# Performance work log

Measured on AMD Instinct MI355X. Metric: run time of the kernel, lower is better.

## Reference

```python
import jax, jax.numpy as jnp
import numpy as np

H_HEADS = 16
STATE_N = 64

def setup_inputs() -> dict:
    key = jax.random.key(0)
    ks = jax.random.split(key, 9)
    B, T, D = 2, 1024, 1024
    H, ch, N = H_HEADS, D // H_HEADS, STATE_N
    inp = jax.random.normal(ks[0], (B, T, D), dtype=jnp.float32)
    # lin_logA params scaled so exp(cumsum(logA)) stays bounded (decaying state)
    W_logA = jax.random.normal(ks[1], (H, 1, ch), dtype=jnp.float32) * 0.01
    b_logA = jnp.full((H, 1), -0.05, dtype=jnp.float32)
    W_XBC = jax.random.normal(ks[3], (H, ch + 2 * N, ch), dtype=jnp.float32) * (1.0 / np.sqrt(ch))
    b_XBC = jax.random.normal(ks[4], (H, ch + 2 * N), dtype=jnp.float32) * 0.02
    W_gate = jax.random.normal(ks[5], (H, ch, ch), dtype=jnp.float32) * (1.0 / np.sqrt(ch))
    b_gate = jax.random.normal(ks[6], (H, ch), dtype=jnp.float32) * 0.02
    W_out = jax.random.normal(ks[7], (D, D), dtype=jnp.float32) * (1.0 / np.sqrt(D))
    b_out = jax.random.normal(ks[8], (D,), dtype=jnp.float32) * 0.02
    return {"inp": inp, "W_logA": W_logA, "b_logA": b_logA, "W_XBC": W_XBC,
            "b_XBC": b_XBC, "W_gate": W_gate, "b_gate": b_gate,
            "W_out": W_out, "b_out": b_out}

def _mamba2_forward(inp, W_logA, b_logA, W_XBC, b_XBC, W_gate, b_gate, W_out, b_out):
    B, T, D = inp.shape
    H, N = H_HEADS, STATE_N
    ch = D // H
    x = inp.reshape(B, T, H, ch)  # B,T,H,ch
    # MultiheadLinear: matmul((H,out,in), x[...,None]) + bias
    logA = jnp.einsum('hoc,bthc->btho', W_logA, x)[..., 0] + b_logA[:, 0]  # B,T,H
    XBC = jax.nn.silu(jnp.einsum('hoc,bthc->btho', W_XBC, x) + b_XBC)     # B,T,H,ch+2N
    X = XBC[..., :ch]                 # B,T,H,ch
    Bm = XBC[..., ch:ch + N]          # B,T,H,N
    Cm = XBC[..., ch + N:]            # B,T,H,N
    # quadratic SSM: A_ss[b,h,i,j] = exp(cum[i]-cum[j]) for j<=i else 0
    cum = jnp.cumsum(jnp.swapaxes(logA, 1, 2), axis=-1)  # B,H,T
    diff = cum[..., :, None] - cum[..., None, :]          # B,H,T,T
    causal = jnp.tril(jnp.ones((T, T), dtype=bool))
    A_ss = jnp.where(causal, jnp.exp(jnp.where(causal, diff, 0.0)), 0.0)  # B,H,T,T
    G = jnp.einsum('bihn,bjhn->bhij', Cm, Bm)             # B,H,T,T (C_i . B_j)
    Y = jnp.einsum('bhij,bjhc->bihc', A_ss * G, X)        # B,T,H,ch
    gate = jnp.einsum('hoc,bthc->btho', W_gate, x) + b_gate
    Yg = (gate * Y).reshape(B, T, D)
    return Yg @ W_out.T + b_out

def reference(inp, W_logA, b_logA, W_XBC, b_XBC, W_gate, b_gate, W_out, b_out):
    return _mamba2_forward(inp, W_logA, b_logA, W_XBC, b_XBC, W_gate, b_gate, W_out, b_out)
```

## Files before the change

### kernel.cpp

```cpp
#include <hip/hip_runtime.h>

typedef unsigned int   u32;
typedef unsigned short u16;
typedef __attribute__((ext_vector_type(8))) short bf16x8;
typedef __attribute__((ext_vector_type(4))) float f32x4;

__device__ __forceinline__ float bfs(u16 u) {
  union { u32 i; float f; } v; v.i = ((u32)u) << 16; return v.f;
}
__device__ __forceinline__ u16 f2bf(float f) {
  union { float f; u32 i; } v; v.f = f;
  u32 r = v.i + 0x7fffu + ((v.i >> 16) & 1u);
  return (u16)(r >> 16);
}
__device__ __forceinline__ ushort4 f2bf4(float4 v) {
  ushort4 p; p.x = f2bf(v.x); p.y = f2bf(v.y); p.z = f2bf(v.z); p.w = f2bf(v.w);
  return p;
}

__global__ __launch_bounds__(256) void k_proj(
    const float* __restrict__ inp,
    const float* __restrict__ W_XBC,  const float* __restrict__ b_XBC,
    const float* __restrict__ W_gate, const float* __restrict__ b_gate,
    const float* __restrict__ W_logA, const float* __restrict__ b_logA,
    const float* __restrict__ Wout, u16* __restrict__ WoutB,
    u16* __restrict__ XsT, u16* __restrict__ Bms, u16* __restrict__ Cms,
    u16* __restrict__ gatesP, float* __restrict__ lexp, float* __restrict__ linv,
    float* __restrict__ decArr, float* __restrict__ G)
{
  int tt = blockIdx.x, h = blockIdx.y;
  int tid = threadIdx.x;
  int w = tid >> 6, l = tid & 63, q = l >> 4, lr = l & 15;
  int m0 = tt * 64;
  int b = m0 >> 10, tl0 = m0 & 1023;
  int bh = b * 16 + h;
  int jt = tt & 15;

  __shared__ u16 Xt[64][72];
  __shared__ u16 Wt[256][72];
  __shared__ float wl[64];
  __shared__ float sg[64];

  {
    int fid = h * 32 + tt;
    const float4* src = (const float4*)Wout + (size_t)fid * 512;
    ushort4* dst = (ushort4*)WoutB + (size_t)fid * 512;
    for (int i = tid; i < 512; i += 256) dst[i] = f2bf4(src[i]);
  }

  if (tid < 64) wl[tid] = W_logA[h * 64 + tid];
#pragma unroll
  for (int i = 0; i < 4; ++i) {
    int f = tid + 256 * i; int r = f >> 4, cq = f & 15;
    float4 xv = *(const float4*)(inp + (size_t)(m0 + r) * 1024 + h * 64 + 4 * cq);
    *(ushort4*)&Xt[r][4 * cq] = f2bf4(xv);
  }
#pragma unroll
  for (int i = 0; i < 16; ++i) {
    int f = tid + 256 * i; int r = f >> 4, cq = f & 15;
    const float* ws = (r < 192) ? (W_XBC + ((size_t)h * 192 + r) * 64)
                                : (W_gate + ((size_t)h * 64 + (r - 192)) * 64);
    *(ushort4*)&Wt[r][4 * cq] = f2bf4(*(const float4*)(ws + 4 * cq));
  }
  __syncthreads();

  bf16x8 af[4][2];
#pragma unroll
  for (int rt = 0; rt < 4; ++rt) {
    af[rt][0] = *(const bf16x8*)&Xt[16 * rt + lr][q * 8];
    af[rt][1] = *(const bf16x8*)&Xt[16 * rt + lr][32 + q * 8];
  }

  f32x4 acc[4][4];
#pragma unroll
  for (int rt = 0; rt < 4; ++rt)
#pragma unroll
    for (int ct = 0; ct < 4; ++ct) acc[rt][ct] = (f32x4){0.f, 0.f, 0.f, 0.f};

#pragma unroll
  for (int ct = 0; ct < 4; ++ct) {
    bf16x8 b0 = *(const bf16x8*)&Wt[64 * w + 16 * ct + lr][q * 8];
    bf16x8 b1 = *(const bf16x8*)&Wt[64 * w + 16 * ct + lr][32 + q * 8];
#pragma unroll
    for (int rt = 0; rt < 4; ++rt) {
      acc[rt][ct] = __builtin_amdgcn_mfma_f32_16x16x32_bf16(af[rt][0], b0, acc[rt][ct], 0, 0, 0);
      acc[rt][ct] = __builtin_amdgcn_mfma_f32_16x16x32_bf16(af[rt][1], b1, acc[rt][ct], 0, 0, 0);
    }
  }

  if (tid < 64) {
    float a = b_logA[h];
#pragma unroll 16
    for (int k = 0; k < 64; ++k) a += bfs(Xt[tid][k]) * wl[k];
    float lv = a;
#pragma unroll
    for (int off = 1; off < 64; off <<= 1) {
      float n = __shfl_up(lv, off, 64);
      if (tid >= off) lv += n;
    }
    float L = __shfl(lv, 63, 64);
    sg[tid] = __expf(L - lv);
    lexp[(size_t)bh * 1024 + tl0 + tid] = __expf(lv);
    linv[(size_t)bh * 1024 + tl0 + tid] = __expf(-lv);
    if (tid == 63) decArr[bh * 16 + jt] = __expf(L);
  }

  if (w < 3) {
#pragma unroll
    for (int ct = 0; ct < 4; ++ct) {
      float bias = b_XBC[h * 192 + 64 * w + 16 * ct + lr];
#pragma unroll
      for (int rt = 0; rt < 4; ++rt)
#pragma unroll
        for (int r = 0; r < 4; ++r) {
          float s = acc[rt][ct][r] + bias;
          acc[rt][ct][r] = s / (1.f + __expf(-s));
        }
    }
  } else {
#pragma unroll
    for (int ct = 0; ct < 4; ++ct) {
      float bias = b_gate[h * 64 + 16 * ct + lr];
#pragma unroll
      for (int rt = 0; rt < 4; ++rt)
#pragma unroll
        for (int r = 0; r < 4; ++r) acc[rt][ct][r] += bias;
    }
  }
  __syncthreads();

  {
#pragma unroll
    for (int ct = 0; ct < 4; ++ct)
#pragma unroll
      for (int rt = 0; rt < 4; ++rt)
#pragma unroll
        for (int r = 0; r < 4; ++r) {
          int t = 16 * rt + 4 * q + r, n = 16 * ct + lr;
          u16 v = f2bf(acc[rt][ct][r]);
          if (w == 0) {
            Wt[n][t] = v;
          } else if (w == 1) {
            Wt[64 + n][t] = v;
            Xt[t][n] = v;
          } else if (w == 2) {
            Wt[128 + t][n] = v;
          } else {
            Wt[192 + t][n] = v;
          }
        }
  }
  __syncthreads();

  {
#pragma unroll
    for (int i = 0; i < 16; ++i) {
      int s = l + 64 * i; int row = s >> 4, cq = s & 15;
      if (w == 0) {
        ushort4 v = *(ushort4*)&Wt[row][4 * cq];
        *(ushort4*)(XsT + ((size_t)bh * 64 + row) * 1024 + tl0 + 4 * cq) = v;
      } else if (w == 1) {
        ushort4 v = *(ushort4*)&Xt[row][4 * cq];
        *(ushort4*)(Bms + ((size_t)bh * 1024 + tl0 + row) * 64 + 4 * cq) = v;
      } else if (w == 2) {
        ushort4 v = *(ushort4*)&Wt[128 + row][4 * cq];
        *(ushort4*)(Cms + ((size_t)bh * 1024 + tl0 + row) * 64 + 4 * cq) = v;
      } else {
        ushort4 v = *(ushort4*)&Wt[192 + row][4 * cq];
        *(ushort4*)(gatesP + ((size_t)bh * 1024 + tl0 + row) * 64 + 4 * cq) = v;
      }
    }
  }

  {
    bf16x8 a0r = *(const bf16x8*)&Wt[16 * w + lr][q * 8];
    bf16x8 a1r = *(const bf16x8*)&Wt[16 * w + lr][32 + q * 8];
    bf16x8 a0, a1;
#pragma unroll
    for (int jj = 0; jj < 8; ++jj) {
      a0[jj] = (short)f2bf(bfs((u16)a0r[jj]) * sg[q * 8 + jj]);
      a1[jj] = (short)f2bf(bfs((u16)a1r[jj]) * sg[32 + q * 8 + jj]);
    }
    f32x4 gacc[4];
#pragma unroll
    for (int nt = 0; nt < 4; ++nt) {
      gacc[nt] = (f32x4){0.f, 0.f, 0.f, 0.f};
      bf16x8 bb0 = *(const bf16x8*)&Wt[64 + 16 * nt + lr][q * 8];
      bf16x8 bb1 = *(const bf16x8*)&Wt[64 + 16 * nt + lr][32 + q * 8];
      gacc[nt] = __builtin_amdgcn_mfma_f32_16x16x32_bf16(a0, bb0, gacc[nt], 0, 0, 0);
      gacc[nt] = __builtin_amdgcn_mfma_f32_16x16x32_bf16(a1, bb1, gacc[nt], 0, 0, 0);
    }
    float* Gt = G + ((size_t)bh * 16 + jt) * 4096;
#pragma unroll
    for (int nt = 0; nt < 4; ++nt)
#pragma unroll
      for (int r = 0; r < 4; ++r)
        Gt[(16 * w + 4 * q + r) * 64 + 16 * nt + lr] = gacc[nt][r];
  }
}

__global__ __launch_bounds__(256) void k_mid(
    const float* __restrict__ G, const float* __restrict__ decArr,
    u16* __restrict__ HpreT)
{
  int cc = blockIdx.x, bh = blockIdx.y;
  int tid = threadIdx.x;
  int e = cc * 256 + tid;
  __shared__ float dsm[16];
  if (tid < 16) dsm[tid] = decArr[bh * 16 + tid];
  __syncthreads();
  const float* Gb = G + (size_t)bh * 16 * 4096 + e;
  float g[16];
#pragma unroll
  for (int jtl = 0; jtl < 16; ++jtl) g[jtl] = Gb[(size_t)jtl * 4096];
  u16* Hb = HpreT + (size_t)bh * 16 * 4096 + e;
  float hst = 0.f;
#pragma unroll
  for (int jtl = 0; jtl < 16; ++jtl) {
    Hb[(size_t)jtl * 4096] = f2bf(hst);
    hst = dsm[jtl] * hst + g[jtl];
  }
}

__global__ __launch_bounds__(256) void k_ssm2(
    const u16* __restrict__ XsT, const u16* __restrict__ Bms,
    const u16* __restrict__ Cms,
    const float* __restrict__ lexp, const float* __restrict__ linv,
    const u16* __restrict__ HpreT, const u16* __restrict__ gatesP,
    u16* __restrict__ Yg)
{
  int it = blockIdx.x, bh = blockIdx.y;
  int b = bh >> 4, h = bh & 15;
  int tid = threadIdx.x;
  int w = tid >> 6, l = tid & 63, q = l >> 4, lr = l & 15;
  int i0 = it * 64;

  __shared__ u16 Cts[64][72];
  __shared__ u16 Bts[64][72];
  __shared__ u16 Xts[64][72];
  __shared__ u16 HTt[64][72];
  __shared__ u16 Sts[64][72];
  __shared__ float ref_[64], cef[64];

  const u16* Xb = XsT + (size_t)bh * 64 * 1024;
  const u16* Bb = Bms + (size_t)bh * 64 * 1024;
  const u16* Cb = Cms + (size_t)bh * 64 * 1024;
  const u16* Hb = HpreT + ((size_t)bh * 16 + it) * 4096;
  const u16* Gb = gatesP + ((size_t)bh * 1024 + i0) * 64;

#pragma unroll
  for (int i = 0; i < 4; ++i) {
    int f = tid + 256 * i; int r = f >> 4, cq = f & 15;
    *(ushort4*)&Xts[r][4 * cq] = *(const ushort4*)(Xb + (size_t)r * 1024 + i0 + 4 * cq);
    *(ushort4*)&HTt[r][4 * cq] = *(const ushort4*)(Hb + r * 64 + 4 * cq);
    *(ushort4*)&Bts[r][4 * cq] = *(const ushort4*)(Bb + (size_t)(i0 + r) * 64 + 4 * cq);
    *(ushort4*)&Cts[r][4 * cq] = *(const ushort4*)(Cb + (size_t)(i0 + r) * 64 + 4 * cq);
  }
  if (tid < 64) {
    ref_[tid] = lexp[(size_t)bh * 1024 + i0 + tid];
    cef[tid]  = linv[(size_t)bh * 1024 + i0 + tid];
  }
  __syncthreads();

  bf16x8 ca0 = *(const bf16x8*)&Cts[16 * w + lr][q * 8];
  bf16x8 ca1 = *(const bf16x8*)&Cts[16 * w + lr][32 + q * 8];

#pragma unroll
  for (int ct = 0; ct < 4; ++ct) {
    f32x4 s = (f32x4){0.f, 0.f, 0.f, 0.f};
    bf16x8 b0 = *(const bf16x8*)&Bts[16 * ct + lr][q * 8];
    bf16x8 b1 = *(const bf16x8*)&Bts[16 * ct + lr][32 + q * 8];
    s = __builtin_amdgcn_mfma_f32_16x16x32_bf16(ca0, b0, s, 0, 0, 0);
    s = __builtin_amdgcn_mfma_f32_16x16x32_bf16(ca1, b1, s, 0, 0, 0);
    int jl = 16 * ct + lr;
    float cj = cef[jl];
#pragma unroll
    for (int r = 0; r < 4; ++r) {
      int il = 16 * w + q * 4 + r;
      float v = (jl > il) ? 0.f : s[r] * ref_[il] * cj;
      Sts[il][jl] = f2bf(v);
    }
  }

  bf16x8 sa0 = *(const bf16x8*)&Sts[16 * w + lr][q * 8];
  bf16x8 sa1 = *(const bf16x8*)&Sts[16 * w + lr][32 + q * 8];
  f32x4 accd[4], acco[4];
#pragma unroll
  for (int ct = 0; ct < 4; ++ct) {
    accd[ct] = (f32x4){0.f, 0.f, 0.f, 0.f};
    acco[ct] = (f32x4){0.f, 0.f, 0.f, 0.f};
    bf16x8 x0 = *(const bf16x8*)&Xts[16 * ct + lr][q * 8];
    bf16x8 x1 = *(const bf16x8*)&Xts[16 * ct + lr][32 + q * 8];
    accd[ct] = __builtin_amdgcn_mfma_f32_16x16x32_bf16(sa0, x0, accd[ct], 0, 0, 0);
    accd[ct] = __builtin_amdgcn_mfma_f32_16x16x32_bf16(sa1, x1, accd[ct], 0, 0, 0);
    bf16x8 h0 = *(const bf16x8*)&HTt[16 * ct + lr][q * 8];
    bf16x8 h1 = *(const bf16x8*)&HTt[16 * ct + lr][32 + q * 8];
    acco[ct] = __builtin_amdgcn_mfma_f32_16x16x32_bf16(ca0, h0, acco[ct], 0, 0, 0);
    acco[ct] = __builtin_amdgcn_mfma_f32_16x16x32_bf16(ca1, h1, acco[ct], 0, 0, 0);
  }

  __syncthreads();

#pragma unroll
  for (int ct = 0; ct < 4; ++ct) {
    int c = 16 * ct + lr;
#pragma unroll
    for (int r = 0; r < 4; ++r) {
      int il = 16 * w + q * 4 + r;
      float y = accd[ct][r] + ref_[il] * acco[ct][r];
      Xts[il][c] = f2bf(y);
    }
  }
  __syncthreads();

#pragma unroll
  for (int i = 0; i < 4; ++i) {
    int f = tid + 256 * i; int r = f >> 4, cq = f & 15;
    ushort4 yv = *(ushort4*)&Xts[r][4 * cq];
    ushort4 gv = *(const ushort4*)(Gb + (size_t)r * 64 + 4 * cq);
    ushort4 o;
    o.x = f2bf(bfs(yv.x) * bfs(gv.x));
    o.y = f2bf(bfs(yv.y) * bfs(gv.y));
    o.z = f2bf(bfs(yv.z) * bfs(gv.z));
    o.w = f2bf(bfs(yv.w) * bfs(gv.w));
    *(ushort4*)(Yg + ((size_t)(b * 1024 + i0 + r)) * 1024 + h * 64 + 4 * cq) = o;
  }
}

__global__ __launch_bounds__(512) void k_out(
    const u16* __restrict__ Yg, const u16* __restrict__ WoutB,
    const float* __restrict__ bout, float* __restrict__ out)
{
  int bm = blockIdx.x, bn = blockIdx.y;
  int tid = threadIdx.x;
  int w = tid >> 6, l = tid & 63, q = l >> 4, lr = l & 15;
  int m0 = bm * 128, d0 = bn * 64;

  __shared__ u16 Yt[128][72];
  __shared__ u16 Wt[64][72];

  f32x4 acc[4];
#pragma unroll
  for (int ct = 0; ct < 4; ++ct) acc[ct] = (f32x4){0.f, 0.f, 0.f, 0.f};

  ushort4 py[4], pw[2];
#pragma unroll
  for (int i = 0; i < 4; ++i) {
    int f = tid + 512 * i; int r = f >> 4, cq = f & 15;
    py[i] = *(const ushort4*)(Yg + (size_t)(m0 + r) * 1024 + 4 * cq);
  }
#pragma unroll
  for (int i = 0; i < 2; ++i) {
    int f = tid + 512 * i; int r = f >> 4, cq = f & 15;
    pw[i] = *(const ushort4*)(WoutB + (size_t)(d0 + r) * 1024 + 4 * cq);
  }

  for (int kt = 0; kt < 16; ++kt) {
    __syncthreads();
#pragma unroll
    for (int i = 0; i < 4; ++i) {
      int f = tid + 512 * i; int r = f >> 4, cq = f & 15;
      *(ushort4*)&Yt[r][4 * cq] = py[i];
    }
#pragma unroll
    for (int i = 0; i < 2; ++i) {
      int f = tid + 512 * i; int r = f >> 4, cq = f & 15;
      *(ushort4*)&Wt[r][4 * cq] = pw[i];
    }
    __syncthreads();

    if (kt < 15) {
      int k1 = (kt + 1) * 64;
#pragma unroll
      for (int i = 0; i < 4; ++i) {
        int f = tid + 512 * i; int r = f >> 4, cq = f & 15;
        py[i] = *(const ushort4*)(Yg + (size_t)(m0 + r) * 1024 + k1 + 4 * cq);
      }
#pragma unroll
      for (int i = 0; i < 2; ++i) {
        int f = tid + 512 * i; int r = f >> 4, cq = f & 15;
        pw[i] = *(const ushort4*)(WoutB + (size_t)(d0 + r) * 1024 + k1 + 4 * cq);
      }
    }

    bf16x8 a0 = *(const bf16x8*)&Yt[16 * w + lr][q * 8];
    bf16x8 a1 = *(const bf16x8*)&Yt[16 * w + lr][32 + q * 8];
#pragma unroll
    for (int ct = 0; ct < 4; ++ct) {
      bf16x8 b0 = *(const bf16x8*)&Wt[16 * ct + lr][q * 8];
      bf16x8 b1 = *(const bf16x8*)&Wt[16 * ct + lr][32 + q * 8];
      acc[ct] = __builtin_amdgcn_mfma_f32_16x16x32_bf16(a0, b0, acc[ct], 0, 0, 0);
      acc[ct] = __builtin_amdgcn_mfma_f32_16x16x32_bf16(a1, b1, acc[ct], 0, 0, 0);
    }
  }

#pragma unroll
  for (int ct = 0; ct < 4; ++ct) {
    int d = d0 + 16 * ct + lr;
    float bo = bout[d];
#pragma unroll
    for (int r = 0; r < 4; ++r) {
      int m = m0 + 16 * w + q * 4 + r;
      out[(size_t)m * 1024 + d] = acc[ct][r] + bo;
    }
  }
}

extern "C" void kernel_launch(void* const* d_in, const int* in_sizes, int n_in,
                              void* d_out, int out_size, void* d_ws, size_t ws_size,
                              hipStream_t stream)
{
  const float* inp   = (const float*)d_in[0];
  const float* WlogA = (const float*)d_in[1];
  const float* blogA = (const float*)d_in[2];
  const float* WXBC  = (const float*)d_in[3];
  const float* bXBC  = (const float*)d_in[4];
  const float* Wgate = (const float*)d_in[5];
  const float* bgate = (const float*)d_in[6];
  const float* Wout  = (const float*)d_in[7];
  const float* bout  = (const float*)d_in[8];
  float* out = (float*)d_out;

  const size_t SZ = (size_t)2 * 16 * 1024 * 64;
  float* lexp   = (float*)d_ws;
  float* linv   = lexp + 32768;
  float* decA   = linv + 32768;
  float* G      = decA + 512;
  u16* base16 = (u16*)(G + (size_t)32 * 16 * 4096);
  u16* XsT    = base16;
  u16* Bms    = XsT + SZ;
  u16* Cms    = Bms + SZ;
  u16* gatesP = Cms + SZ;
  u16* Yg     = gatesP + SZ;
  u16* WoutB  = Yg + SZ;
  u16* HpreT  = WoutB + 1024 * 1024;

  k_proj<<<dim3(32, 16), 256, 0, stream>>>(inp, WXBC, bXBC, Wgate, bgate,
                                           WlogA, blogA, Wout, WoutB,
                                           XsT, Bms, Cms, gatesP,
                                           lexp, linv, decA, G);
  k_mid<<<dim3(16, 32), 256, 0, stream>>>(G, decA, HpreT);
  k_ssm2<<<dim3(16, 32), 256, 0, stream>>>(XsT, Bms, Cms, lexp, linv,
                                           HpreT, gatesP, Yg);
  k_out<<<dim3(16, 16), 512, 0, stream>>>(Yg, WoutB, bout, out);
}
```

Before: 125.4 us.

## Fuse all four kernels into one persistent kernel with grid barriers

Merges projection, chunk-state scan, SSM and output GEMM into a single 512-block kernel separated by atomic grid-wide barriers. XBC, B, C and gate tiles stay in shared memory between phases instead of round-tripping through global buffers, and three extra launches are removed. The output GEMM is retiled to 64x64 per 256-thread block to match the fused grid. This relies on all 512 blocks being co-resident (launch_bounds 256,2) and adds spin-wait barrier overhead plus a memset launch.

```diff
diff --git a/kernel.cpp b/kernel.cpp
--- a/kernel.cpp
+++ b/kernel.cpp
@@ -18,28 +18,43 @@
   return p;
 }
 
-__global__ __launch_bounds__(256) void k_proj(
+#define NBLK 512u
+
+__device__ __forceinline__ void gridbar(u32* cnt, int idx) {
+  __threadfence();
+  __syncthreads();
+  if (threadIdx.x == 0) {
+    __hip_atomic_fetch_add(&cnt[idx], 1u, __ATOMIC_ACQ_REL, __HIP_MEMORY_SCOPE_AGENT);
+    while (__hip_atomic_load(&cnt[idx], __ATOMIC_ACQUIRE, __HIP_MEMORY_SCOPE_AGENT) < NBLK) {}
+  }
+  __syncthreads();
+  __threadfence();
+}
+
+__global__ __launch_bounds__(256, 2) void k_fused(
     const float* __restrict__ inp,
     const float* __restrict__ W_XBC,  const float* __restrict__ b_XBC,
     const float* __restrict__ W_gate, const float* __restrict__ b_gate,
     const float* __restrict__ W_logA, const float* __restrict__ b_logA,
-    const float* __restrict__ Wout, u16* __restrict__ WoutB,
-    u16* __restrict__ XsT, u16* __restrict__ Bms, u16* __restrict__ Cms,
-    u16* __restrict__ gatesP, float* __restrict__ lexp, float* __restrict__ linv,
-    float* __restrict__ decArr, float* __restrict__ G)
+    const float* __restrict__ Wout,   const float* __restrict__ bout,
+    u32* __restrict__ bar,
+    u16* __restrict__ WoutB, float* __restrict__ decArr,
+    float* __restrict__ G, u16* __restrict__ HpreT,
+    u16* __restrict__ Yg, float* __restrict__ out)
 {
-  int tt = blockIdx.x, h = blockIdx.y;
-  int tid = threadIdx.x;
-  int w = tid >> 6, l = tid & 63, q = l >> 4, lr = l & 15;
-  int m0 = tt * 64;
-  int b = m0 >> 10, tl0 = m0 & 1023;
-  int bh = b * 16 + h;
-  int jt = tt & 15;
+  const int tt = blockIdx.x, h = blockIdx.y;
+  const int tid = threadIdx.x;
+  const int w = tid >> 6, l = tid & 63, q = l >> 4, lr = l & 15;
+  const int m0 = tt * 64;
+  const int b = tt >> 4;
+  const int bh = b * 16 + h;
+  const int it = tt & 15;
 
   __shared__ u16 Xt[64][72];
   __shared__ u16 Wt[256][72];
   __shared__ float wl[64];
   __shared__ float sg[64];
+  __shared__ float ref_[64], cef[64];
 
   {
     int fid = h * 32 + tt;
@@ -64,72 +79,72 @@
   }
   __syncthreads();
 
-  bf16x8 af[4][2];
-#pragma unroll
-  for (int rt = 0; rt < 4; ++rt) {
-    af[rt][0] = *(const bf16x8*)&Xt[16 * rt + lr][q * 8];
-    af[rt][1] = *(const bf16x8*)&Xt[16 * rt + lr][32 + q * 8];
-  }
-
-  f32x4 acc[4][4];
-#pragma unroll
-  for (int rt = 0; rt < 4; ++rt)
-#pragma unroll
-    for (int ct = 0; ct < 4; ++ct) acc[rt][ct] = (f32x4){0.f, 0.f, 0.f, 0.f};
-
-#pragma unroll
-  for (int ct = 0; ct < 4; ++ct) {
-    bf16x8 b0 = *(const bf16x8*)&Wt[64 * w + 16 * ct + lr][q * 8];
-    bf16x8 b1 = *(const bf16x8*)&Wt[64 * w + 16 * ct + lr][32 + q * 8];
+  {
+    bf16x8 af[4][2];
 #pragma unroll
     for (int rt = 0; rt < 4; ++rt) {
-      acc[rt][ct] = __builtin_amdgcn_mfma_f32_16x16x32_bf16(af[rt][0], b0, acc[rt][ct], 0, 0, 0);
-      acc[rt][ct] = __builtin_amdgcn_mfma_f32_16x16x32_bf16(af[rt][1], b1, acc[rt][ct], 0, 0, 0);
-    }
-  }
-
-  if (tid < 64) {
-    float a = b_logA[h];
+      af[rt][0] = *(const bf16x8*)&Xt[16 * rt + lr][q * 8];
+      af[rt][1] = *(const bf16x8*)&Xt[16 * rt + lr][32 + q * 8];
+    }
+
+    f32x4 acc[4][4];
+#pragma unroll
+    for (int rt = 0; rt < 4; ++rt)
+#pragma unroll
+      for (int ct = 0; ct < 4; ++ct) acc[rt][ct] = (f32x4){0.f, 0.f, 0.f, 0.f};
+
+#pragma unroll
+    for (int ct = 0; ct < 4; ++ct) {
+      bf16x8 b0 = *(const bf16x8*)&Wt[64 * w + 16 * ct + lr][q * 8];
+      bf16x8 b1 = *(const bf16x8*)&Wt[64 * w + 16 * ct + lr][32 + q * 8];
+#pragma unroll
+      for (int rt = 0; rt < 4; ++rt) {
+        acc[rt][ct] = __builtin_amdgcn_mfma_f32_16x16x32_bf16(af[rt][0], b0, acc[rt][ct], 0, 0, 0);
+        acc[rt][ct] = __builtin_amdgcn_mfma_f32_16x16x32_bf16(af[rt][1], b1, acc[rt][ct], 0, 0, 0);
+      }
+    }
+
+    if (tid < 64) {
+      float a = b_logA[h];
 #pragma unroll 16
-    for (int k = 0; k < 64; ++k) a += bfs(Xt[tid][k]) * wl[k];
-    float lv = a;
-#pragma unroll
-    for (int off = 1; off < 64; off <<= 1) {
-      float n = __shfl_up(lv, off, 64);
-      if (tid >= off) lv += n;
-    }
-    float L = __shfl(lv, 63, 64);
-    sg[tid] = __expf(L - lv);
-    lexp[(size_t)bh * 1024 + tl0 + tid] = __expf(lv);
-    linv[(size_t)bh * 1024 + tl0 + tid] = __expf(-lv);
-    if (tid == 63) decArr[bh * 16 + jt] = __expf(L);
-  }
-
-  if (w < 3) {
-#pragma unroll
-    for (int ct = 0; ct < 4; ++ct) {
-      float bias = b_XBC[h * 192 + 64 * w + 16 * ct + lr];
-#pragma unroll
-      for (int rt = 0; rt < 4; ++rt)
-#pragma unroll
-        for (int r = 0; r < 4; ++r) {
-          float s = acc[rt][ct][r] + bias;
-          acc[rt][ct][r] = s / (1.f + __expf(-s));
-        }
-    }
-  } else {
-#pragma unroll
-    for (int ct = 0; ct < 4; ++ct) {
-      float bias = b_gate[h * 64 + 16 * ct + lr];
-#pragma unroll
-      for (int rt = 0; rt < 4; ++rt)
-#pragma unroll
-        for (int r = 0; r < 4; ++r) acc[rt][ct][r] += bias;
-    }
-  }
-  __syncthreads();
-
-  {
+      for (int k = 0; k < 64; ++k) a += bfs(Xt[tid][k]) * wl[k];
+      float lv = a;
+#pragma unroll
+      for (int off = 1; off < 64; off <<= 1) {
+        float n = __shfl_up(lv, off, 64);
+        if (tid >= off) lv += n;
+      }
+      float L = __shfl(lv, 63, 64);
+      sg[tid]   = __expf(L - lv);
+      ref_[tid] = __expf(lv);
+      cef[tid]  = __expf(-lv);
+      if (tid == 63) decArr[bh * 16 + it] = __expf(L);
+    }
+
+    if (w < 3) {
+#pragma unroll
+      for (int ct = 0; ct < 4; ++ct) {
+        float bias = b_XBC[h * 192 + 64 * w + 16 * ct + lr];
+#pragma unroll
+        for (int rt = 0; rt < 4; ++rt)
+#pragma unroll
+          for (int r = 0; r < 4; ++r) {
+            float s = acc[rt][ct][r] + bias;
+            acc[rt][ct][r] = s / (1.f + __expf(-s));
+          }
+      }
+    } else {
+#pragma unroll
+      for (int ct = 0; ct < 4; ++ct) {
+        float bias = b_gate[h * 64 + 16 * ct + lr];
+#pragma unroll
+        for (int rt = 0; rt < 4; ++rt)
+#pragma unroll
+          for (int r = 0; r < 4; ++r) acc[rt][ct][r] += bias;
+      }
+    }
+    __syncthreads();
+
 #pragma unroll
     for (int ct = 0; ct < 4; ++ct)
 #pragma unroll
@@ -149,259 +164,190 @@
             Wt[192 + t][n] = v;
           }
         }
-  }
-  __syncthreads();
-
-  {
-#pragma unroll
-    for (int i = 0; i < 16; ++i) {
-      int s = l + 64 * i; int row = s >> 4, cq = s & 15;
-      if (w == 0) {
-        ushort4 v = *(ushort4*)&Wt[row][4 * cq];
-        *(ushort4*)(XsT + ((size_t)bh * 64 + row) * 1024 + tl0 + 4 * cq) = v;
-      } else if (w == 1) {
-        ushort4 v = *(ushort4*)&Xt[row][4 * cq];
-        *(ushort4*)(Bms + ((size_t)bh * 1024 + tl0 + row) * 64 + 4 * cq) = v;
-      } else if (w == 2) {
-        ushort4 v = *(ushort4*)&Wt[128 + row][4 * cq];
-        *(ushort4*)(Cms + ((size_t)bh * 1024 + tl0 + row) * 64 + 4 * cq) = v;
-      } else {
-        ushort4 v = *(ushort4*)&Wt[192 + row][4 * cq];
-        *(ushort4*)(gatesP + ((size_t)bh * 1024 + tl0 + row) * 64 + 4 * cq) = v;
-      }
-    }
-  }
-
-  {
-    bf16x8 a0r = *(const bf16x8*)&Wt[16 * w + lr][q * 8];
-    bf16x8 a1r = *(const bf16x8*)&Wt[16 * w + lr][32 + q * 8];
-    bf16x8 a0, a1;
-#pragma unroll
-    for (int jj = 0; jj < 8; ++jj) {
-      a0[jj] = (short)f2bf(bfs((u16)a0r[jj]) * sg[q * 8 + jj]);
-      a1[jj] = (short)f2bf(bfs((u16)a1r[jj]) * sg[32 + q * 8 + jj]);
-    }
-    f32x4 gacc[4];
-#pragma unroll
-    for (int nt = 0; nt < 4; ++nt) {
-      gacc[nt] = (f32x4){0.f, 0.f, 0.f, 0.f};
-      bf16x8 bb0 = *(const bf16x8*)&Wt[64 + 16 * nt + lr][q * 8];
-      bf16x8 bb1 = *(const bf16x8*)&Wt[64 + 16 * nt + lr][32 + q * 8];
-      gacc[nt] = __builtin_amdgcn_mfma_f32_16x16x32_bf16(a0, bb0, gacc[nt], 0, 0, 0);
-      gacc[nt] = __builtin_amdgcn_mfma_f32_16x16x32_bf16(a1, bb1, gacc[nt], 0, 0, 0);
-    }
-    float* Gt = G + ((size_t)bh * 16 + jt) * 4096;
-#pragma unroll
-    for (int nt = 0; nt < 4; ++nt)
-#pragma unroll
-      for (int r = 0; r < 4; ++r)
-        Gt[(16 * w + 4 * q + r) * 64 + 16 * nt + lr] = gacc[nt][r];
-  }
-}
-
-__global__ __launch_bounds__(256) void k_mid(
-    const float* __restrict__ G, const float* __restrict__ decArr,
-    u16* __restrict__ HpreT)
-{
-  int cc = blockIdx.x, bh = blockIdx.y;
-  int tid = threadIdx.x;
-  int e = cc * 256 + tid;
-  __shared__ float dsm[16];
-  if (tid < 16) dsm[tid] = decArr[bh * 16 + tid];
-  __syncthreads();
-  const float* Gb = G + (size_t)bh * 16 * 4096 + e;
-  float g[16];
-#pragma unroll
-  for (int jtl = 0; jtl < 16; ++jtl) g[jtl] = Gb[(size_t)jtl * 4096];
-  u16* Hb = HpreT + (size_t)bh * 16 * 4096 + e;
-  float hst = 0.f;
-#pragma unroll
-  for (int jtl = 0; jtl < 16; ++jtl) {
-    Hb[(size_t)jtl * 4096] = f2bf(hst);
-    hst = dsm[jtl] * hst + g[jtl];
-  }
-}
-
-__global__ __launch_bounds__(256) void k_ssm2(
-    const u16* __restrict__ XsT, const u16* __restrict__ Bms,
-    const u16* __restrict__ Cms,
-    const float* __restrict__ lexp, const float* __restrict__ linv,
-    const u16* __restrict__ HpreT, const u16* __restrict__ gatesP,
-    u16* __restrict__ Yg)
-{
-  int it = blockIdx.x, bh = blockIdx.y;
-  int b = bh >> 4, h = bh & 15;
-  int tid = threadIdx.x;
-  int w = tid >> 6, l = tid & 63, q = l >> 4, lr = l & 15;
-  int i0 = it * 64;
-
-  __shared__ u16 Cts[64][72];
-  __shared__ u16 Bts[64][72];
-  __shared__ u16 Xts[64][72];
-  __shared__ u16 HTt[64][72];
-  __shared__ u16 Sts[64][72];
-  __shared__ float ref_[64], cef[64];
-
-  const u16* Xb = XsT + (size_t)bh * 64 * 1024;
-  const u16* Bb = Bms + (size_t)bh * 64 * 1024;
-  const u16* Cb = Cms + (size_t)bh * 64 * 1024;
-  const u16* Hb = HpreT + ((size_t)bh * 16 + it) * 4096;
-  const u16* Gb = gatesP + ((size_t)bh * 1024 + i0) * 64;
-
-#pragma unroll
-  for (int i = 0; i < 4; ++i) {
-    int f = tid + 256 * i; int r = f >> 4, cq = f & 15;
-    *(ushort4*)&Xts[r][4 * cq] = *(const ushort4*)(Xb + (size_t)r * 1024 + i0 + 4 * cq);
-    *(ushort4*)&HTt[r][4 * cq] = *(const ushort4*)(Hb + r * 64 + 4 * cq);
-    *(ushort4*)&Bts[r][4 * cq] = *(const ushort4*)(Bb + (size_t)(i0 + r) * 64 + 4 * cq);
-    *(ushort4*)&Cts[r][4 * cq] = *(const ushort4*)(Cb + (size_t)(i0 + r) * 64 + 4 * cq);
-  }
-  if (tid < 64) {
-    ref_[tid] = lexp[(size_t)bh * 1024 + i0 + tid];
-    cef[tid]  = linv[(size_t)bh * 1024 + i0 + tid];
-  }
-  __syncthreads();
-
-  bf16x8 ca0 = *(const bf16x8*)&Cts[16 * w + lr][q * 8];
-  bf16x8 ca1 = *(const bf16x8*)&Cts[16 * w + lr][32 + q * 8];
-
-#pragma unroll
-  for (int ct = 0; ct < 4; ++ct) {
-    f32x4 s = (f32x4){0.f, 0.f, 0.f, 0.f};
-    bf16x8 b0 = *(const bf16x8*)&Bts[16 * ct + lr][q * 8];
-    bf16x8 b1 = *(const bf16x8*)&Bts[16 * ct + lr][32 + q * 8];
-    s = __builtin_amdgcn_mfma_f32_16x16x32_bf16(ca0, b0, s, 0, 0, 0);
-    s = __builtin_amdgcn_mfma_f32_16x16x32_bf16(ca1, b1, s, 0, 0, 0);
-    int jl = 16 * ct + lr;
-    float cj = cef[jl];
-#pragma unroll
-    for (int r = 0; r < 4; ++r) {
-      int il = 16 * w + q * 4 + r;
-      float v = (jl > il) ? 0.f : s[r] * ref_[il] * cj;
-      Sts[il][jl] = f2bf(v);
-    }
-  }
-
-  bf16x8 sa0 = *(const bf16x8*)&Sts[16 * w + lr][q * 8];
-  bf16x8 sa1 = *(const bf16x8*)&Sts[16 * w + lr][32 + q * 8];
-  f32x4 accd[4], acco[4];
-#pragma unroll
-  for (int ct = 0; ct < 4; ++ct) {
-    accd[ct] = (f32x4){0.f, 0.f, 0.f, 0.f};
-    acco[ct] = (f32x4){0.f, 0.f, 0.f, 0.f};
-    bf16x8 x0 = *(const bf16x8*)&Xts[16 * ct + lr][q * 8];
-    bf16x8 x1 = *(const bf16x8*)&Xts[16 * ct + lr][32 + q * 8];
-    accd[ct] = __builtin_amdgcn_mfma_f32_16x16x32_bf16(sa0, x0, accd[ct], 0, 0, 0);
-    accd[ct] = __builtin_amdgcn_mfma_f32_16x16x32_bf16(sa1, x1, accd[ct], 0, 0, 0);
-    bf16x8 h0 = *(const bf16x8*)&HTt[16 * ct + lr][q * 8];
-    bf16x8 h1 = *(const bf16x8*)&HTt[16 * ct + lr][32 + q * 8];
-    acco[ct] = __builtin_amdgcn_mfma_f32_16x16x32_bf16(ca0, h0, acco[ct], 0, 0, 0);
-    acco[ct] = __builtin_amdgcn_mfma_f32_16x16x32_bf16(ca1, h1, acco[ct], 0, 0, 0);
-  }
-
-  __syncthreads();
-
-#pragma unroll
-  for (int ct = 0; ct < 4; ++ct) {
-    int c = 16 * ct + lr;
-#pragma unroll
-    for (int r = 0; r < 4; ++r) {
-      int il = 16 * w + q * 4 + r;
-      float y = accd[ct][r] + ref_[il] * acco[ct][r];
-      Xts[il][c] = f2bf(y);
-    }
-  }
-  __syncthreads();
-
-#pragma unroll
-  for (int i = 0; i < 4; ++i) {
-    int f = tid + 256 * i; int r = f >> 4, cq = f & 15;
-    ushort4 yv = *(ushort4*)&Xts[r][4 * cq];
-    ushort4 gv = *(const ushort4*)(Gb + (size_t)r * 64 + 4 * cq);
-    ushort4 o;
-    o.x = f2bf(bfs(yv.x) * bfs(gv.x));
-    o.y = f2bf(bfs(yv.y) * bfs(gv.y));
-    o.z = f2bf(bfs(yv.z) * bfs(gv.z));
-    o.w = f2bf(bfs(yv.w) * bfs(gv.w));
-    *(ushort4*)(Yg + ((size_t)(b * 1024 + i0 + r)) * 1024 + h * 64 + 4 * cq) = o;
-  }
-}
-
-__global__ __launch_bounds__(512) void k_out(
-    const u16* __restrict__ Yg, const u16* __restrict__ WoutB,
-    const float* __restrict__ bout, float* __restrict__ out)
-{
-  int bm = blockIdx.x, bn = blockIdx.y;
-  int tid = threadIdx.x;
-  int w = tid >> 6, l = tid & 63, q = l >> 4, lr = l & 15;
-  int m0 = bm * 128, d0 = bn * 64;
-
-  __shared__ u16 Yt[128][72];
-  __shared__ u16 Wt[64][72];
-
-  f32x4 acc[4];
-#pragma unroll
-  for (int ct = 0; ct < 4; ++ct) acc[ct] = (f32x4){0.f, 0.f, 0.f, 0.f};
-
-  ushort4 py[4], pw[2];
-#pragma unroll
-  for (int i = 0; i < 4; ++i) {
-    int f = tid + 512 * i; int r = f >> 4, cq = f & 15;
-    py[i] = *(const ushort4*)(Yg + (size_t)(m0 + r) * 1024 + 4 * cq);
-  }
-#pragma unroll
-  for (int i = 0; i < 2; ++i) {
-    int f = tid + 512 * i; int r = f >> 4, cq = f & 15;
-    pw[i] = *(const ushort4*)(WoutB + (size_t)(d0 + r) * 1024 + 4 * cq);
-  }
-
-  for (int kt = 0; kt < 16; ++kt) {
-    __syncthreads();
+    __syncthreads();
+
+    {
+      bf16x8 a0r = *(const bf16x8*)&Wt[16 * w + lr][q * 8];
+      bf16x8 a1r = *(const bf16x8*)&Wt[16 * w + lr][32 + q * 8];
+      bf16x8 a0, a1;
+#pragma unroll
+      for (int jj = 0; jj < 8; ++jj) {
+        a0[jj] = (short)f2bf(bfs((u16)a0r[jj]) * sg[q * 8 + jj]);
+        a1[jj] = (short)f2bf(bfs((u16)a1r[jj]) * sg[32 + q * 8 + jj]);
+      }
+      f32x4 gacc[4];
+#pragma unroll
+      for (int nt = 0; nt < 4; ++nt) {
+        gacc[nt] = (f32x4){0.f, 0.f, 0.f, 0.f};
+        bf16x8 bb0 = *(const bf16x8*)&Wt[64 + 16 * nt + lr][q * 8];
+        bf16x8 bb1 = *(const bf16x8*)&Wt[64 + 16 * nt + lr][32 + q * 8];
+        gacc[nt] = __builtin_amdgcn_mfma_f32_16x16x32_bf16(a0, bb0, gacc[nt], 0, 0, 0);
+        gacc[nt] = __builtin_amdgcn_mfma_f32_16x16x32_bf16(a1, bb1, gacc[nt], 0, 0, 0);
+      }
+      float* Gt = G + ((size_t)bh * 16 + it) * 4096;
+#pragma unroll
+      for (int nt = 0; nt < 4; ++nt)
+#pragma unroll
+        for (int r = 0; r < 4; ++r)
+          Gt[(16 * w + 4 * q + r) * 64 + 16 * nt + lr] = gacc[nt][r];
+    }
+  }
+
+  gridbar(bar, 0);
+
+  {
+    int fb = (h << 5) | tt;
+    int bh2 = fb >> 4;
+    int e = ((fb & 15) << 8) + tid;
+    if (tid < 16) wl[tid] = decArr[bh2 * 16 + tid];
+    __syncthreads();
+    const float* Gb = G + (size_t)bh2 * 16 * 4096 + e;
+    u16* Hb = HpreT + (size_t)bh2 * 16 * 4096 + e;
+    float gv[16];
+#pragma unroll
+    for (int j = 0; j < 16; ++j) gv[j] = Gb[(size_t)j * 4096];
+    float hst = 0.f;
+#pragma unroll
+    for (int j = 0; j < 16; ++j) {
+      Hb[(size_t)j * 4096] = f2bf(hst);
+      hst = wl[j] * hst + gv[j];
+    }
+  }
+
+  gridbar(bar, 1);
+
+  {
+    const u16* Hb = HpreT + ((size_t)bh * 16 + it) * 4096;
+
+    u16 (*Xts)[72] = (u16 (*)[72])&Wt[0];
+    u16 (*Sts)[72] = (u16 (*)[72])&Wt[64];
+    u16 (*Cts)[72] = (u16 (*)[72])&Wt[128];
+    u16 (*Gts)[72] = (u16 (*)[72])&Wt[192];
+
+    bf16x8 ca0 = *(const bf16x8*)&Cts[16 * w + lr][q * 8];
+    bf16x8 ca1 = *(const bf16x8*)&Cts[16 * w + lr][32 + q * 8];
+
+#pragma unroll
+    for (int ct = 0; ct < 4; ++ct) {
+      f32x4 s = (f32x4){0.f, 0.f, 0.f, 0.f};
+      bf16x8 b0 = *(const bf16x8*)&Xt[16 * ct + lr][q * 8];
+      bf16x8 b1 = *(const bf16x8*)&Xt[16 * ct + lr][32 + q * 8];
+      s = __builtin_amdgcn_mfma_f32_16x16x32_bf16(ca0, b0, s, 0, 0, 0);
+      s = __builtin_amdgcn_mfma_f32_16x16x32_bf16(ca1, b1, s, 0, 0, 0);
+      int jl = 16 * ct + lr;
+      float cj = cef[jl];
+#pragma unroll
+      for (int r = 0; r < 4; ++r) {
+        int il = 16 * w + q * 4 + r;
+        float v = (jl > il) ? 0.f : s[r] * ref_[il] * cj;
+        Sts[il][jl] = f2bf(v);
+      }
+    }
+
+    bf16x8 sa0 = *(const bf16x8*)&Sts[16 * w + lr][q * 8];
+    bf16x8 sa1 = *(const bf16x8*)&Sts[16 * w + lr][32 + q * 8];
+    f32x4 accd[4], acco[4];
+#pragma unroll
+    for (int ct = 0; ct < 4; ++ct) {
+      accd[ct] = (f32x4){0.f, 0.f, 0.f, 0.f};
+      acco[ct] = (f32x4){0.f, 0.f, 0.f, 0.f};
+      bf16x8 x0 = *(const bf16x8*)&Xts[16 * ct + lr][q * 8];
+      bf16x8 x1 = *(const bf16x8*)&Xts[16 * ct + lr][32 + q * 8];
+      accd[ct] = __builtin_amdgcn_mfma_f32_16x16x32_bf16(sa0, x0, accd[ct], 0, 0, 0);
+      accd[ct] = __builtin_amdgcn_mfma_f32_16x16x32_bf16(sa1, x1, accd[ct], 0, 0, 0);
+      bf16x8 h0 = *(const bf16x8*)(Hb + (size_t)(16 * ct + lr) * 64 + q * 8);
+      bf16x8 h1 = *(const bf16x8*)(Hb + (size_t)(16 * ct + lr) * 64 + 32 + q * 8);
+      acco[ct] = __builtin_amdgcn_mfma_f32_16x16x32_bf16(ca0, h0, acco[ct], 0, 0, 0);
+      acco[ct] = __builtin_amdgcn_mfma_f32_16x16x32_bf16(ca1, h1, acco[ct], 0, 0, 0);
+    }
+
+    __syncthreads();
+
+#pragma unroll
+    for (int ct = 0; ct < 4; ++ct) {
+      int c = 16 * ct + lr;
+#pragma unroll
+      for (int r = 0; r < 4; ++r) {
+        int il = 16 * w + q * 4 + r;
+        float y = accd[ct][r] + ref_[il] * acco[ct][r];
+        Xts[il][c] = f2bf(y);
+      }
+    }
+    __syncthreads();
+
 #pragma unroll
     for (int i = 0; i < 4; ++i) {
-      int f = tid + 512 * i; int r = f >> 4, cq = f & 15;
-      *(ushort4*)&Yt[r][4 * cq] = py[i];
-    }
-#pragma unroll
-    for (int i = 0; i < 2; ++i) {
-      int f = tid + 512 * i; int r = f >> 4, cq = f & 15;
-      *(ushort4*)&Wt[r][4 * cq] = pw[i];
-    }
-    __syncthreads();
-
-    if (kt < 15) {
-      int k1 = (kt + 1) * 64;
+      int f = tid + 256 * i; int r = f >> 4, cq = f & 15;
+      ushort4 yv = *(ushort4*)&Xts[r][4 * cq];
+      ushort4 gv = *(ushort4*)&Gts[r][4 * cq];
+      ushort4 o;
+      o.x = f2bf(bfs(yv.x) * bfs(gv.x));
+      o.y = f2bf(bfs(yv.y) * bfs(gv.y));
+      o.z = f2bf(bfs(yv.z) * bfs(gv.z));
+      o.w = f2bf(bfs(yv.w) * bfs(gv.w));
+      *(ushort4*)(Yg + ((size_t)(m0 + r)) * 1024 + h * 64 + 4 * cq) = o;
+    }
+  }
+
+  gridbar(bar, 2);
+
+  {
+    const int d0 = h * 64;
+    u16 (*Yt)[72]  = Xt;
+    u16 (*Wtt)[72] = (u16 (*)[72])&Wt[0];
+
+    f32x4 oacc[4];
+#pragma unroll
+    for (int ct = 0; ct < 4; ++ct) oacc[ct] = (f32x4){0.f, 0.f, 0.f, 0.f};
+
+    ushort4 py[4], pw[4];
+#pragma unroll
+    for (int i = 0; i < 4; ++i) {
+      int f = tid + 256 * i; int r = f >> 4, cq = f & 15;
+      py[i] = *(const ushort4*)(Yg + (size_t)(m0 + r) * 1024 + 4 * cq);
+      pw[i] = *(const ushort4*)(WoutB + (size_t)(d0 + r) * 1024 + 4 * cq);
+    }
+
+    for (int kt = 0; kt < 16; ++kt) {
+      __syncthreads();
 #pragma unroll
       for (int i = 0; i < 4; ++i) {
-        int f = tid + 512 * i; int r = f >> 4, cq = f & 15;
-        py[i] = *(const ushort4*)(Yg + (size_t)(m0 + r) * 1024 + k1 + 4 * cq);
-      }
-#pragma unroll
-      for (int i = 0; i < 2; ++i) {
-        int f = tid + 512 * i; int r = f >> 4, cq = f & 15;
-        pw[i] = *(const ushort4*)(WoutB + (size_t)(d0 + r) * 1024 + k1 + 4 * cq);
-      }
-    }
-
-    bf16x8 a0 = *(const bf16x8*)&Yt[16 * w + lr][q * 8];
-    bf16x8 a1 = *(const bf16x8*)&Yt[16 * w + lr][32 + q * 8];
-#pragma unroll
-    for (int ct = 0; ct < 4; ++ct) {
-      bf16x8 b0 = *(const bf16x8*)&Wt[16 * ct + lr][q * 8];
-      bf16x8 b1 = *(const bf16x8*)&Wt[16 * ct + lr][32 + q * 8];
-      acc[ct] = __builtin_amdgcn_mfma_f32_16x16x32_bf16(a0, b0, acc[ct], 0, 0, 0);
-      acc[ct] = __builtin_amdgcn_mfma_f32_16x16x32_bf16(a1, b1, acc[ct], 0, 0, 0);
-    }
-  }
-
-#pragma unroll
-  for (int ct = 0; ct < 4; ++ct) {
-    int d = d0 + 16 * ct + lr;
-    float bo = bout[d];
-#pragma unroll
-    for (int r = 0; r < 4; ++r) {
-      int m = m0 + 16 * w + q * 4 + r;
-      out[(size_t)m * 1024 + d] = acc[ct][r] + bo;
+        int f = tid + 256 * i; int r = f >> 4, cq = f & 15;
+        *(ushort4*)&Yt[r][4 * cq]  = py[i];
+        *(ushort4*)&Wtt[r][4 * cq] = pw[i];
+      }
+      __syncthreads();
+
+      if (kt < 15) {
+        int k1 = (kt + 1) * 64;
+#pragma unroll
+        for (int i = 0; i < 4; ++i) {
+          int f = tid + 256 * i; int r = f >> 4, cq = f & 15;
+          py[i] = *(const ushort4*)(Yg + (size_t)(m0 + r) * 1024 + k1 + 4 * cq);
+          pw[i] = *(const ushort4*)(WoutB + (size_t)(d0 + r) * 1024 + k1 + 4 * cq);
+        }
+      }
+
+      bf16x8 a0 = *(const bf16x8*)&Yt[16 * w + lr][q * 8];
+      bf16x8 a1 = *(const bf16x8*)&Yt[16 * w + lr][32 + q * 8];
+#pragma unroll
+      for (int ct = 0; ct < 4; ++ct) {
+        bf16x8 b0 = *(const bf16x8*)&Wtt[16 * ct + lr][q * 8];
+        bf16x8 b1 = *(const bf16x8*)&Wtt[16 * ct + lr][32 + q * 8];
+        oacc[ct] = __builtin_amdgcn_mfma_f32_16x16x32_bf16(a0, b0, oacc[ct], 0, 0, 0);
+        oacc[ct] = __builtin_amdgcn_mfma_f32_16x16x32_bf16(a1, b1, oacc[ct], 0, 0, 0);
+      }
+    }
+
+#pragma unroll
+    for (int ct = 0; ct < 4; ++ct) {
+      int d = d0 + 16 * ct + lr;
+      float bo = bout[d];
+#pragma unroll
+      for (int r = 0; r < 4; ++r) {
+        int m = m0 + 16 * w + q * 4 + r;
+        out[(size_t)m * 1024 + d] = oacc[ct][r] + bo;
+      }
     }
   }
 }
@@ -421,26 +367,16 @@
   const float* bout  = (const float*)d_in[8];
   float* out = (float*)d_out;
 
-  const size_t SZ = (size_t)2 * 16 * 1024 * 64;
-  float* lexp   = (float*)d_ws;
-  float* linv   = lexp + 32768;
-  float* decA   = linv + 32768;
-  float* G      = decA + 512;
-  u16* base16 = (u16*)(G + (size_t)32 * 16 * 4096);
-  u16* XsT    = base16;
-  u16* Bms    = XsT + SZ;
-  u16* Cms    = Bms + SZ;
-  u16* gatesP = Cms + SZ;
-  u16* Yg     = gatesP + SZ;
-  u16* WoutB  = Yg + SZ;
-  u16* HpreT  = WoutB + 1024 * 1024;
-
-  k_proj<<<dim3(32, 16), 256, 0, stream>>>(inp, WXBC, bXBC, Wgate, bgate,
-                                           WlogA, blogA, Wout, WoutB,
-                                           XsT, Bms, Cms, gatesP,
-                                           lexp, linv, decA, G);
-  k_mid<<<dim3(16, 32), 256, 0, stream>>>(G, decA, HpreT);
-  k_ssm2<<<dim3(16, 32), 256, 0, stream>>>(XsT, Bms, Cms, lexp, linv,
-                                           HpreT, gatesP, Yg);
-  k_out<<<dim3(16, 16), 512, 0, stream>>>(Yg, WoutB, bout, out);
-}
+  u32*   bar   = (u32*)d_ws;
+  float* decA  = (float*)((char*)d_ws + 256);
+  float* G     = decA + 512;
+  u16*   WoutB = (u16*)(G + (size_t)32 * 16 * 4096);
+  u16*   HpreT = WoutB + (size_t)1024 * 1024;
+  u16*   Yg    = HpreT + (size_t)2 * 1024 * 1024;
+
+  hipMemsetAsync(bar, 0, 256, stream);
+
+  k_fused<<<dim3(32, 16, 1), dim3(256, 1, 1), 0, stream>>>(
+      inp, WXBC, bXBC, Wgate, bgate, WlogA, blogA, Wout, bout,
+      bar, WoutB, decA, G, HpreT, Yg, out);
+}
```

Measured after the change: 445.8 us. 3.56x slower.
